# Optimization experiments

Hardware: AMD Instinct MI355X
Metric: run time of the kernel (lower is better)

## Reference

```python
import jax, jax.numpy as jnp
import numpy as np

B, S, E, H = 4, 4096, 768, 8
D = E // H  # head_dim = 96


def setup_inputs() -> dict:
    key = jax.random.key(0)
    ks = jax.random.split(key, 9)
    std = 1.0 / np.sqrt(E)
    return {
        "values": jax.random.normal(ks[0], (B, S, E), dtype=jnp.float32),
        "keys": jax.random.normal(ks[1], (B, S, E), dtype=jnp.float32),
        "query": jax.random.normal(ks[2], (B, S, E), dtype=jnp.float32),
        "mask": jax.random.randint(ks[3], (B, S, 1, 1), 0, 2, dtype=jnp.int32),
        "Wv": jax.random.normal(ks[4], (E, E), dtype=jnp.float32) * std,
        "Wk": jax.random.normal(ks[5], (E, E), dtype=jnp.float32) * std,
        "Wq": jax.random.normal(ks[6], (E, E), dtype=jnp.float32) * std,
        "Wo": jax.random.normal(ks[7], (E, E), dtype=jnp.float32) * std,
        "bo": jax.random.normal(ks[8], (E,), dtype=jnp.float32) * std,
    }


def reference(values, keys, query, mask, Wv, Wk, Wq, Wo, bo):
    b, s, e = query.shape
    h, d = H, e // H
    scale = e ** 0.5

    def split(x, W):
        # Linear (no bias) then view to [b, s, h, d] and permute to [b, h, s, d]
        return (x @ W.T).reshape(b, s, h, d).transpose(0, 2, 1, 3)

    v = split(values, Wv)   # [b, h, s, d]
    k = split(keys, Wk)     # [b, h, s, d]
    q = split(query, Wq)    # [b, h, s, d]

    # Faithful to torch.einsum('nqhd,nkhd->nhqk', q, k) with q,k laid out as
    # [b, h, s, d]: this contracts over d with s batched, producing a per-token
    # head-gram matrix att[b, s, i, j] = sum_d q[b,i,s,d] * k[b,j,s,d].
    att = jnp.einsum('bisd,bjsd->bsij', q, k)          # [b, s, h, h]
    att = jnp.where(mask == 0, jnp.float32(-1e20), att)
    att = jax.nn.softmax(att / scale, axis=3)

    # torch.einsum('nhql,nlhd->nqhd', att, v) with att [b,s,h,h], v [b,h,s,d]:
    # out[b, i, s, d] = sum_j att[b,s,i,j] * v[b,j,s,d]  -> [b, h, s, d]
    out = jnp.einsum('bsij,bjsd->bisd', att, v)        # [b, h, s, d]
    out = out.reshape(b, s, h * d)                      # row-major, matches torch .reshape
    return out @ Wo.T + bo
```

## Files before the change

kernel.cpp:

```cpp
#include <hip/hip_runtime.h>
#include <hip/hip_bf16.h>
#include <cstdint>


typedef unsigned short u16;
typedef short bf16x8 __attribute__((ext_vector_type(8)));
typedef float f32x4 __attribute__((ext_vector_type(4)));

#define B_  4
#define S_  4096
#define E_  768
#define H_  8
#define D_  96
#define T_  (B_*S_)
#define BM_ 256
#define BN_ 192

static __device__ __forceinline__ u16 f2bf(float f) {
  unsigned u = __builtin_bit_cast(unsigned, f);
  u += 0x7fffu + ((u >> 16) & 1u);
  return (u16)(u >> 16);
}
static __device__ __forceinline__ unsigned pk2(float lo, float hi) {
  return (unsigned)f2bf(lo) | ((unsigned)f2bf(hi) << 16);
}
static __device__ __forceinline__ float bflo(unsigned u) {
  return __builtin_bit_cast(float, u << 16);
}
static __device__ __forceinline__ float bfhi(unsigned u) {
  return __builtin_bit_cast(float, u & 0xffff0000u);
}

__global__ __launch_bounds__(256) void conv_bf16(
    const float* __restrict__ src, u16* __restrict__ dst)
{
  const int i = blockIdx.x * 256 + threadIdx.x;
  const float4 v = ((const float4*)src)[i];
  uint2 w;
  w.x = pk2(v.x, v.y);
  w.y = pk2(v.z, v.w);
  ((uint2*)dst)[i] = w;
}

__global__ __launch_bounds__(256) void conv_w(
    const float* __restrict__ w0, const float* __restrict__ w1,
    const float* __restrict__ w2, const float* __restrict__ w3,
    u16* __restrict__ dst)
{
  const int bpw = (E_ * E_ / 4) / 256;
  const int which = blockIdx.x / bpw;
  const float* src = which == 0 ? w0 : which == 1 ? w1 : which == 2 ? w2 : w3;
  const int i = (blockIdx.x - which * bpw) * 256 + threadIdx.x;
  const float4 v = ((const float4*)src)[i];
  uint2 w;
  w.x = pk2(v.x, v.y);
  w.y = pk2(v.z, v.w);
  ((uint2*)(dst + (size_t)which * E_ * E_))[i] = w;
}


#define GLOAD(SRC, DST)                                                        \
  __builtin_amdgcn_global_load_lds(                                            \
      (const __attribute__((address_space(1))) void*)(SRC),                    \
      (__attribute__((address_space(3))) void*)(DST), 16, 0, 0)

#define SA(BUF, I, KT) GLOAD(sA[I] + (KT), &lA[BUF][(((I) << 3) + wave) * 512])
#define SB(BUF, I, KT) GLOAD(sB[I] + (KT), &lB[BUF][(((I) << 3) + wave) * 512])

#define RDA(BUF, MH, KK, M)                                                    \
  (*(const bf16x8*)&lA[BUF][((wr << 7) + ((MH) << 6) + ((M) << 4) + l15) * 64 +\
      (((((KK) << 2) + l4) ^ (((MH) << 6) + ((M) << 4) + l15 ? ((((MH) << 6) + ((M) << 4) + l15) & 7) : 0)) << 3)])

#define MFMA12(MB)                                                             \
  {                                                                            \
    _Pragma("unroll")                                                          \
    for (int m_ = 0; m_ < 4; ++m_) {                                           \
      acc[(MB) + m_][0] = __builtin_amdgcn_mfma_f32_16x16x32_bf16(a[m_], b[0], acc[(MB) + m_][0], 0, 0, 0); \
      acc[(MB) + m_][1] = __builtin_amdgcn_mfma_f32_16x16x32_bf16(a[m_], b[1], acc[(MB) + m_][1], 0, 0, 0); \
      acc[(MB) + m_][2] = __builtin_amdgcn_mfma_f32_16x16x32_bf16(a[m_], b[2], acc[(MB) + m_][2], 0, 0, 0); \
    }                                                                          \
  }

template<bool OUT_F32, bool BIAS>
__global__ __launch_bounds__(512, 2) void gemm_big(
    const u16* __restrict__ A, const u16* __restrict__ Wt,
    const float* __restrict__ bias, void* __restrict__ Cv)
{
  __shared__ u16 lA[2][256 * 64];
  __shared__ u16 lB[2][192 * 64];
  const int tid = threadIdx.x, wave = tid >> 6, lane = tid & 63;
  const int wr = wave >> 2, wcn = wave & 3;
  const int wg = ((blockIdx.x & 7) << 5) + (blockIdx.x >> 3);
  const int tM = (wg >> 2) << 8, tN = (wg & 3) * BN_;
  const int l15 = lane & 15, l4 = lane >> 4;
  const int srow = lane >> 3;
  const int sg   = (lane & 7) ^ srow;

  const u16* sA[4];
  const u16* sB[3];
#pragma unroll
  for (int i = 0; i < 4; ++i)
    sA[i] = A + (size_t)(tM + (((i << 3) + wave) << 3) + srow) * E_ + (sg << 3);
#pragma unroll
  for (int i = 0; i < 3; ++i)
    sB[i] = Wt + (size_t)(tN + (((i << 3) + wave) << 3) + srow) * E_ + (sg << 3);

  f32x4 acc[8][3] = {};

#pragma unroll
  for (int i = 0; i < 4; ++i) SA(0, i, 0);
#pragma unroll
  for (int i = 0; i < 3; ++i) SB(0, i, 0);
  asm volatile("s_waitcnt vmcnt(0)" ::: "memory");
  __builtin_amdgcn_s_barrier();

  for (int t = 0; t < 12; ++t) {
    const int cur = t & 1, nxt = cur ^ 1;
    const int ktn = (t + 1) << 6;
    const bool pf = (t < 11);
    bf16x8 a[4], b[3];

#pragma unroll
    for (int m = 0; m < 4; ++m) {
      const int row = (wr << 7) + (m << 4) + l15;
      a[m] = *(const bf16x8*)&lA[cur][row * 64 + ((l4 ^ (row & 7)) << 3)];
    }
#pragma unroll
    for (int n = 0; n < 3; ++n) {
      const int row = wcn * 48 + (n << 4) + l15;
      b[n] = *(const bf16x8*)&lB[cur][row * 64 + ((l4 ^ (row & 7)) << 3)];
    }
    if (pf) { SA(nxt, 0, ktn); SA(nxt, 1, ktn); SA(nxt, 2, ktn); }
    __builtin_amdgcn_s_barrier();
    __builtin_amdgcn_s_setprio(1);
    MFMA12(0);
    __builtin_amdgcn_s_setprio(0);
    __builtin_amdgcn_s_barrier();

#pragma unroll
    for (int m = 0; m < 4; ++m) {
      const int row = (wr << 7) + 64 + (m << 4) + l15;
      a[m] = *(const bf16x8*)&lA[cur][row * 64 + ((l4 ^ (row & 7)) << 3)];
    }
    if (pf) { SA(nxt, 3, ktn); SB(nxt, 0, ktn); }
    __builtin_amdgcn_s_barrier();
    __builtin_amdgcn_s_setprio(1);
    MFMA12(4);
    __builtin_amdgcn_s_setprio(0);
    __builtin_amdgcn_s_barrier();

#pragma unroll
    for (int m = 0; m < 4; ++m) {
      const int row = (wr << 7) + (m << 4) + l15;
      a[m] = *(const bf16x8*)&lA[cur][row * 64 + (((4 + l4) ^ (row & 7)) << 3)];
    }
#pragma unroll
    for (int n = 0; n < 3; ++n) {
      const int row = wcn * 48 + (n << 4) + l15;
      b[n] = *(const bf16x8*)&lB[cur][row * 64 + (((4 + l4) ^ (row & 7)) << 3)];
    }
    if (pf) { SB(nxt, 1, ktn); SB(nxt, 2, ktn); }
    __builtin_amdgcn_s_barrier();
    __builtin_amdgcn_s_setprio(1);
    MFMA12(0);
    __builtin_amdgcn_s_setprio(0);
    __builtin_amdgcn_s_barrier();

#pragma unroll
    for (int m = 0; m < 4; ++m) {
      const int row = (wr << 7) + 64 + (m << 4) + l15;
      a[m] = *(const bf16x8*)&lA[cur][row * 64 + (((4 + l4) ^ (row & 7)) << 3)];
    }
    __builtin_amdgcn_s_barrier();
    __builtin_amdgcn_s_setprio(1);
    MFMA12(4);
    __builtin_amdgcn_s_setprio(0);
    if (pf) asm volatile("s_waitcnt vmcnt(0)" ::: "memory");
    __builtin_amdgcn_s_barrier();
  }

  const int cr = l4 << 2;
#pragma unroll
  for (int m = 0; m < 8; ++m) {
#pragma unroll
    for (int n = 0; n < 3; ++n) {
      const int row = tM + (wr << 7) + (m << 4) + cr;
      const int col = tN + wcn * 48 + (n << 4) + l15;
      const float badd = BIAS ? bias[col] : 0.f;
#pragma unroll
      for (int r = 0; r < 4; ++r) {
        const float val = acc[m][n][r] + badd;
        if constexpr (OUT_F32)
          ((float*)Cv)[(size_t)(row + r) * E_ + col] = val;
        else
          ((u16*)Cv)[(size_t)(row + r) * E_ + col] = f2bf(val);
      }
    }
  }
}

__global__ __launch_bounds__(256) void attn_tok(
    const u16* __restrict__ Q, const u16* __restrict__ K,
    const u16* __restrict__ V, const int* __restrict__ mask,
    u16* __restrict__ O)
{
  __shared__ float pl[4][8][8];
  const int tid = threadIdx.x, wave = tid >> 6, lane = tid & 63;
  const int t = blockIdx.x * 4 + wave;
  const int s = t & (S_ - 1);
  const int b = t >> 12;
  const int i = lane >> 3, j = lane & 7;

  const uint4* qp = (const uint4*)(Q + (size_t)t * E_ + i * D_);
  const uint4* kp = (const uint4*)(K + (size_t)t * E_ + j * D_);
  float acc = 0.f;
#pragma unroll
  for (int it = 0; it < 12; ++it) {
    const uint4 qv = qp[it], kv = kp[it];
    acc += bflo(qv.x) * bflo(kv.x) + bfhi(qv.x) * bfhi(kv.x);
    acc += bflo(qv.y) * bflo(kv.y) + bfhi(qv.y) * bfhi(kv.y);
    acc += bflo(qv.z) * bflo(kv.z) + bfhi(qv.z) * bfhi(kv.z);
    acc += bflo(qv.w) * bflo(kv.w) + bfhi(qv.w) * bfhi(kv.w);
  }
  float sv = (mask[t] == 0) ? -1e20f : acc;
  sv *= 0.03608439182435161f;
  float mx = sv;
  mx = fmaxf(mx, __shfl_xor(mx, 1));
  mx = fmaxf(mx, __shfl_xor(mx, 2));
  mx = fmaxf(mx, __shfl_xor(mx, 4));
  const float e = __expf(sv - mx);
  float sm = e;
  sm += __shfl_xor(sm, 1);
  sm += __shfl_xor(sm, 2);
  sm += __shfl_xor(sm, 4);
  pl[wave][i][j] = e / sm;
  __syncthreads();

  const int i2 = lane >> 3, db = lane & 7;
  float o[12] = {};
#pragma unroll
  for (int jj = 0; jj < 8; ++jj) {
    const float pj = pl[wave][i2][jj];
    const uint2* vp = (const uint2*)(V + (size_t)t * E_ + jj * D_ + db * 12);
    const uint2 v0 = vp[0], v1 = vp[1], v2 = vp[2];
    o[0]  += pj * bflo(v0.x);  o[1]  += pj * bfhi(v0.x);
    o[2]  += pj * bflo(v0.y);  o[3]  += pj * bfhi(v0.y);
    o[4]  += pj * bflo(v1.x);  o[5]  += pj * bfhi(v1.x);
    o[6]  += pj * bflo(v1.y);  o[7]  += pj * bfhi(v1.y);
    o[8]  += pj * bflo(v2.x);  o[9]  += pj * bfhi(v2.x);
    o[10] += pj * bflo(v2.y);  o[11] += pj * bfhi(v2.y);
  }
  const size_t row = (size_t)b * S_ + 512 * i2 + (s >> 3);
  u16* op = O + row * E_ + 96 * (s & 7) + db * 12;
  uint2 w0, w1, w2;
  w0.x = pk2(o[0], o[1]);
  w0.y = pk2(o[2], o[3]);
  w1.x = pk2(o[4], o[5]);
  w1.y = pk2(o[6], o[7]);
  w2.x = pk2(o[8], o[9]);
  w2.y = pk2(o[10], o[11]);
  ((uint2*)op)[0] = w0;
  ((uint2*)op)[1] = w1;
  ((uint2*)op)[2] = w2;
}

extern "C" void kernel_launch(void* const* d_in, const int* in_sizes, int n_in,
                              void* d_out, int out_size, void* d_ws, size_t ws_size,
                              hipStream_t stream)
{
  const float* values = (const float*)d_in[0];
  const float* keys   = (const float*)d_in[1];
  const float* query  = (const float*)d_in[2];
  const int*   mask   = (const int*)d_in[3];
  const float* Wv = (const float*)d_in[4];
  const float* Wk = (const float*)d_in[5];
  const float* Wq = (const float*)d_in[6];
  const float* Wo = (const float*)d_in[7];
  const float* bo = (const float*)d_in[8];

  const size_t TE = (size_t)T_ * E_;
  const size_t EE = (size_t)E_ * E_;
  u16* Qb = (u16*)d_ws;
  u16* Kb = Qb + TE;
  u16* Vb = Kb + TE;
  u16* Xt = Vb + TE;
  u16* Wb = Xt + TE;

  dim3 gg(T_ / BM_ * (E_ / BN_));
  dim3 gc(TE / 4 / 256);

  conv_w<<<dim3(4 * (E_ * E_ / 4) / 256), dim3(256), 0, stream>>>(Wq, Wk, Wv, Wo, Wb);

  conv_bf16<<<gc, dim3(256), 0, stream>>>(query, Xt);
  gemm_big<false, false><<<gg, dim3(512), 0, stream>>>(Xt, Wb + 0 * EE, nullptr, Qb);
  conv_bf16<<<gc, dim3(256), 0, stream>>>(keys, Xt);
  gemm_big<false, false><<<gg, dim3(512), 0, stream>>>(Xt, Wb + 1 * EE, nullptr, Kb);
  conv_bf16<<<gc, dim3(256), 0, stream>>>(values, Xt);
  gemm_big<false, false><<<gg, dim3(512), 0, stream>>>(Xt, Wb + 2 * EE, nullptr, Vb);

  attn_tok<<<dim3(T_ / 4), dim3(256), 0, stream>>>(Qb, Kb, Vb, mask, Xt );

  gemm_big<true, true><<<gg, dim3(512), 0, stream>>>(Xt , Wb + 3 * EE, bo, (float*)d_out);
}
```

Before: 184.7 us.

## Fuse fp32-to-bf16 activation conversion into projection GEMM A-tile loads

Removes the three standalone conv_bf16 passes over query/keys/values. The projection GEMMs now read fp32 activations into registers, convert them with v_cvt_pk_bf16_f32 and write swizzled bf16 into LDS. This avoids writing and re-reading a bf16 copy of each input through global memory. In exchange, the A prefetch goes through registers instead of direct global-to-LDS loads, adding register pressure and VALU/LDS-store work inside the pipelined loop.

```diff
diff --git a/kernel.cpp b/kernel.cpp
--- a/kernel.cpp
+++ b/kernel.cpp
@@ -24,22 +24,16 @@
 static __device__ __forceinline__ unsigned pk2(float lo, float hi) {
   return (unsigned)f2bf(lo) | ((unsigned)f2bf(hi) << 16);
 }
+static __device__ __forceinline__ unsigned cvtpk(float lo, float hi) {
+  unsigned r;
+  asm("v_cvt_pk_bf16_f32 %0, %1, %2" : "=v"(r) : "v"(lo), "v"(hi));
+  return r;
+}
 static __device__ __forceinline__ float bflo(unsigned u) {
   return __builtin_bit_cast(float, u << 16);
 }
 static __device__ __forceinline__ float bfhi(unsigned u) {
   return __builtin_bit_cast(float, u & 0xffff0000u);
-}
-
-__global__ __launch_bounds__(256) void conv_bf16(
-    const float* __restrict__ src, u16* __restrict__ dst)
-{
-  const int i = blockIdx.x * 256 + threadIdx.x;
-  const float4 v = ((const float4*)src)[i];
-  uint2 w;
-  w.x = pk2(v.x, v.y);
-  w.y = pk2(v.z, v.w);
-  ((uint2*)dst)[i] = w;
 }
 
 __global__ __launch_bounds__(256) void conv_w(
@@ -67,9 +61,24 @@
 #define SA(BUF, I, KT) GLOAD(sA[I] + (KT), &lA[BUF][(((I) << 3) + wave) * 512])
 #define SB(BUF, I, KT) GLOAD(sB[I] + (KT), &lB[BUF][(((I) << 3) + wave) * 512])
 
-#define RDA(BUF, MH, KK, M)                                                    \
-  (*(const bf16x8*)&lA[BUF][((wr << 7) + ((MH) << 6) + ((M) << 4) + l15) * 64 +\
-      (((((KK) << 2) + l4) ^ (((MH) << 6) + ((M) << 4) + l15 ? ((((MH) << 6) + ((M) << 4) + l15) & 7) : 0)) << 3)])
+#define A_ISSUE(KT)                                                            \
+  {                                                                            \
+    _Pragma("unroll")                                                          \
+    for (int w_ = 0; w_ < 8; ++w_)                                             \
+      av[w_] = *(const float4*)(agp + (KT) + (w_ << 2));                       \
+  }
+#define A_WRITE(BUF)                                                           \
+  {                                                                            \
+    _Pragma("unroll")                                                          \
+    for (int w_ = 0; w_ < 4; ++w_) {                                           \
+      uint4 q_;                                                                \
+      q_.x = cvtpk(av[2 * w_].x, av[2 * w_].y);                                \
+      q_.y = cvtpk(av[2 * w_].z, av[2 * w_].w);                                \
+      q_.z = cvtpk(av[2 * w_ + 1].x, av[2 * w_ + 1].y);                        \
+      q_.w = cvtpk(av[2 * w_ + 1].z, av[2 * w_ + 1].w);                        \
+      *(uint4*)&lA[BUF][ar * 64 + ((((ah << 2) + w_) ^ (ar & 7)) << 3)] = q_;  \
+    }                                                                          \
+  }
 
 #define MFMA12(MB)                                                             \
   {                                                                            \
@@ -81,9 +90,9 @@
     }                                                                          \
   }
 
-template<bool OUT_F32, bool BIAS>
+template<bool A_F32, bool OUT_F32, bool BIAS>
 __global__ __launch_bounds__(512, 2) void gemm_big(
-    const u16* __restrict__ A, const u16* __restrict__ Wt,
+    const void* __restrict__ Av, const u16* __restrict__ Wt,
     const float* __restrict__ bias, void* __restrict__ Cv)
 {
   __shared__ u16 lA[2][256 * 64];
@@ -96,23 +105,37 @@
   const int srow = lane >> 3;
   const int sg   = (lane & 7) ^ srow;
 
+  const u16* A16 = (const u16*)Av;
+  const float* A32 = (const float*)Av;
+
   const u16* sA[4];
   const u16* sB[3];
 #pragma unroll
-  for (int i = 0; i < 4; ++i)
-    sA[i] = A + (size_t)(tM + (((i << 3) + wave) << 3) + srow) * E_ + (sg << 3);
-#pragma unroll
   for (int i = 0; i < 3; ++i)
     sB[i] = Wt + (size_t)(tN + (((i << 3) + wave) << 3) + srow) * E_ + (sg << 3);
+  if constexpr (!A_F32) {
+#pragma unroll
+    for (int i = 0; i < 4; ++i)
+      sA[i] = A16 + (size_t)(tM + (((i << 3) + wave) << 3) + srow) * E_ + (sg << 3);
+  }
+  const int ar = tid >> 1, ah = tid & 1;
+  const float* agp = A32 + (size_t)(tM + ar) * E_ + (ah << 5);
 
   f32x4 acc[8][3] = {};
-
-#pragma unroll
-  for (int i = 0; i < 4; ++i) SA(0, i, 0);
-#pragma unroll
-  for (int i = 0; i < 3; ++i) SB(0, i, 0);
-  asm volatile("s_waitcnt vmcnt(0)" ::: "memory");
-  __builtin_amdgcn_s_barrier();
+  float4 av[8];
+
+  if constexpr (A_F32) {
+    A_ISSUE(0);
+#pragma unroll
+    for (int i = 0; i < 3; ++i) SB(0, i, 0);
+    A_WRITE(0);
+  } else {
+#pragma unroll
+    for (int i = 0; i < 4; ++i) SA(0, i, 0);
+#pragma unroll
+    for (int i = 0; i < 3; ++i) SB(0, i, 0);
+  }
+  __syncthreads();
 
   for (int t = 0; t < 12; ++t) {
     const int cur = t & 1, nxt = cur ^ 1;
@@ -130,7 +153,10 @@
       const int row = wcn * 48 + (n << 4) + l15;
       b[n] = *(const bf16x8*)&lB[cur][row * 64 + ((l4 ^ (row & 7)) << 3)];
     }
-    if (pf) { SA(nxt, 0, ktn); SA(nxt, 1, ktn); SA(nxt, 2, ktn); }
+    if (pf) {
+      if constexpr (A_F32) { A_ISSUE(ktn); }
+      else { SA(nxt, 0, ktn); SA(nxt, 1, ktn); SA(nxt, 2, ktn); }
+    }
     __builtin_amdgcn_s_barrier();
     __builtin_amdgcn_s_setprio(1);
     MFMA12(0);
@@ -142,7 +168,10 @@
       const int row = (wr << 7) + 64 + (m << 4) + l15;
       a[m] = *(const bf16x8*)&lA[cur][row * 64 + ((l4 ^ (row & 7)) << 3)];
     }
-    if (pf) { SA(nxt, 3, ktn); SB(nxt, 0, ktn); }
+    if (pf) {
+      if constexpr (A_F32) { SB(nxt, 0, ktn); SB(nxt, 1, ktn); SB(nxt, 2, ktn); }
+      else { SA(nxt, 3, ktn); SB(nxt, 0, ktn); }
+    }
     __builtin_amdgcn_s_barrier();
     __builtin_amdgcn_s_setprio(1);
     MFMA12(4);
@@ -159,7 +188,9 @@
       const int row = wcn * 48 + (n << 4) + l15;
       b[n] = *(const bf16x8*)&lB[cur][row * 64 + (((4 + l4) ^ (row & 7)) << 3)];
     }
-    if (pf) { SB(nxt, 1, ktn); SB(nxt, 2, ktn); }
+    if (pf) {
+      if constexpr (!A_F32) { SB(nxt, 1, ktn); SB(nxt, 2, ktn); }
+    }
     __builtin_amdgcn_s_barrier();
     __builtin_amdgcn_s_setprio(1);
     MFMA12(0);
@@ -175,7 +206,13 @@
     __builtin_amdgcn_s_setprio(1);
     MFMA12(4);
     __builtin_amdgcn_s_setprio(0);
-    if (pf) asm volatile("s_waitcnt vmcnt(0)" ::: "memory");
+    if (pf) {
+      if constexpr (A_F32) {
+        A_WRITE(nxt);
+        asm volatile("s_waitcnt lgkmcnt(0)" ::: "memory");
+      }
+      asm volatile("s_waitcnt vmcnt(0)" ::: "memory");
+    }
     __builtin_amdgcn_s_barrier();
   }
 
@@ -283,22 +320,18 @@
   u16* Qb = (u16*)d_ws;
   u16* Kb = Qb + TE;
   u16* Vb = Kb + TE;
-  u16* Xt = Vb + TE;
-  u16* Wb = Xt + TE;
+  u16* O2 = Vb + TE;
+  u16* Wb = O2 + TE;
 
   dim3 gg(T_ / BM_ * (E_ / BN_));
-  dim3 gc(TE / 4 / 256);
 
   conv_w<<<dim3(4 * (E_ * E_ / 4) / 256), dim3(256), 0, stream>>>(Wq, Wk, Wv, Wo, Wb);
 
-  conv_bf16<<<gc, dim3(256), 0, stream>>>(query, Xt);
-  gemm_big<false, false><<<gg, dim3(512), 0, stream>>>(Xt, Wb + 0 * EE, nullptr, Qb);
-  conv_bf16<<<gc, dim3(256), 0, stream>>>(keys, Xt);
-  gemm_big<false, false><<<gg, dim3(512), 0, stream>>>(Xt, Wb + 1 * EE, nullptr, Kb);
-  conv_bf16<<<gc, dim3(256), 0, stream>>>(values, Xt);
-  gemm_big<false, false><<<gg, dim3(512), 0, stream>>>(Xt, Wb + 2 * EE, nullptr, Vb);
-
-  attn_tok<<<dim3(T_ / 4), dim3(256), 0, stream>>>(Qb, Kb, Vb, mask, Xt );
-
-  gemm_big<true, true><<<gg, dim3(512), 0, stream>>>(Xt , Wb + 3 * EE, bo, (float*)d_out);
-}
+  gemm_big<true, false, false><<<gg, dim3(512), 0, stream>>>(query,  Wb + 0 * EE, nullptr, Qb);
+  gemm_big<true, false, false><<<gg, dim3(512), 0, stream>>>(keys,   Wb + 1 * EE, nullptr, Kb);
+  gemm_big<true, false, false><<<gg, dim3(512), 0, stream>>>(values, Wb + 2 * EE, nullptr, Vb);
+
+  attn_tok<<<dim3(T_ / 4), dim3(256), 0, stream>>>(Qb, Kb, Vb, mask, O2);
+
+  gemm_big<false, true, true><<<gg, dim3(512), 0, stream>>>(O2, Wb + 3 * EE, bo, (float*)d_out);
+}
```

Result: slower. 216.0 us (+16.9%).

## Rewrite projection GEMM with 256x256 tiles, quadrant pipelining and LDS-staged bf16 epilogue

Applied to the files above, without the earlier changes.

Replaces the 256x192 GEMM tile with a 256x256 tile split into four 128x128 quadrants, each wave computing 64x32 per quadrant. Global-to-LDS loads are staggered across quadrants so the next k-step's halves arrive while MFMAs run. For bf16 outputs the accumulators are staged through swizzled LDS and written as 16-byte coalesced rows instead of scattered 2-byte stores. The larger tile raises arithmetic intensity but cuts the grid to 192 blocks, which may underfill the GPU and leave CUs idle.

```diff
diff --git a/kernel.cpp b/kernel.cpp
--- a/kernel.cpp
+++ b/kernel.cpp
@@ -13,8 +13,6 @@
 #define H_  8
 #define D_  96
 #define T_  (B_*S_)
-#define BM_ 256
-#define BN_ 192
 
 static __device__ __forceinline__ u16 f2bf(float f) {
   unsigned u = __builtin_bit_cast(unsigned, f);
@@ -64,137 +62,147 @@
       (const __attribute__((address_space(1))) void*)(SRC),                    \
       (__attribute__((address_space(3))) void*)(DST), 16, 0, 0)
 
-#define SA(BUF, I, KT) GLOAD(sA[I] + (KT), &lA[BUF][(((I) << 3) + wave) * 512])
-#define SB(BUF, I, KT) GLOAD(sB[I] + (KT), &lB[BUF][(((I) << 3) + wave) * 512])
-
-#define RDA(BUF, MH, KK, M)                                                    \
-  (*(const bf16x8*)&lA[BUF][((wr << 7) + ((MH) << 6) + ((M) << 4) + l15) * 64 +\
-      (((((KK) << 2) + l4) ^ (((MH) << 6) + ((M) << 4) + l15 ? ((((MH) << 6) + ((M) << 4) + l15) & 7) : 0)) << 3)])
-
-#define MFMA12(MB)                                                             \
+#define STG_A(HALF, T)                                                         \
+  {                                                                            \
+    const int b_ = (T) & 1;                                                    \
+    GLOAD(Abase + (size_t)(tM + (HALF)*128 + (wave<<3) + srow8) * E_ + ((T)<<6) + sgo, \
+          &lds[(b_*2 + (HALF)) * 8192 + ((wave*64 + lane) << 3)]);             \
+    GLOAD(Abase + (size_t)(tM + (HALF)*128 + 64 + (wave<<3) + srow8) * E_ + ((T)<<6) + sgo, \
+          &lds[(b_*2 + (HALF)) * 8192 + (((8 + wave)*64 + lane) << 3)]);       \
+  }
+#define STG_B(HALF, T)                                                         \
+  {                                                                            \
+    const int b_ = (T) & 1;                                                    \
+    GLOAD(Wbase + (size_t)(tN + (HALF)*128 + (wave<<3) + srow8) * E_ + ((T)<<6) + sgo, \
+          &lds[32768 + (b_*2 + (HALF)) * 8192 + ((wave*64 + lane) << 3)]);     \
+    GLOAD(Wbase + (size_t)(tN + (HALF)*128 + 64 + (wave<<3) + srow8) * E_ + ((T)<<6) + sgo, \
+          &lds[32768 + (b_*2 + (HALF)) * 8192 + (((8 + wave)*64 + lane) << 3)]); \
+  }
+
+#define RD_A(DST, BUF, MH, KK)                                                 \
   {                                                                            \
     _Pragma("unroll")                                                          \
     for (int m_ = 0; m_ < 4; ++m_) {                                           \
-      acc[(MB) + m_][0] = __builtin_amdgcn_mfma_f32_16x16x32_bf16(a[m_], b[0], acc[(MB) + m_][0], 0, 0, 0); \
-      acc[(MB) + m_][1] = __builtin_amdgcn_mfma_f32_16x16x32_bf16(a[m_], b[1], acc[(MB) + m_][1], 0, 0, 0); \
-      acc[(MB) + m_][2] = __builtin_amdgcn_mfma_f32_16x16x32_bf16(a[m_], b[2], acc[(MB) + m_][2], 0, 0, 0); \
+      const int hr_ = (wr << 6) + (m_ << 4) + l15;                             \
+      DST[m_] = *(const bf16x8*)&lds[((BUF)*2 + (MH)) * 8192 + hr_ * 64 +      \
+                                     (((((KK) << 2) + l4) ^ (hr_ & 7)) << 3)]; \
     }                                                                          \
   }
+#define RD_B(DST, BUF, NH, KK)                                                 \
+  {                                                                            \
+    _Pragma("unroll")                                                          \
+    for (int n_ = 0; n_ < 2; ++n_) {                                           \
+      const int hr_ = (wcn << 5) + (n_ << 4) + l15;                            \
+      DST[n_] = *(const bf16x8*)&lds[32768 + ((BUF)*2 + (NH)) * 8192 + hr_ * 64 + \
+                                     (((((KK) << 2) + l4) ^ (hr_ & 7)) << 3)]; \
+    }                                                                          \
+  }
+
+#define MFMA16(MH, NH, B0N, B1N)                                               \
+  {                                                                            \
+    __builtin_amdgcn_s_setprio(1);                                             \
+    _Pragma("unroll")                                                          \
+    for (int m_ = 0; m_ < 4; ++m_) {                                           \
+      _Pragma("unroll")                                                        \
+      for (int n_ = 0; n_ < 2; ++n_) {                                         \
+        acc[MH][NH][m_][n_] = __builtin_amdgcn_mfma_f32_16x16x32_bf16(a0[m_], B0N[n_], acc[MH][NH][m_][n_], 0, 0, 0); \
+        acc[MH][NH][m_][n_] = __builtin_amdgcn_mfma_f32_16x16x32_bf16(a1[m_], B1N[n_], acc[MH][NH][m_][n_], 0, 0, 0); \
+      }                                                                        \
+    }                                                                          \
+    __builtin_amdgcn_s_setprio(0);                                             \
+  }
 
 template<bool OUT_F32, bool BIAS>
-__global__ __launch_bounds__(512, 2) void gemm_big(
-    const u16* __restrict__ A, const u16* __restrict__ Wt,
+__global__ __launch_bounds__(512, 2) void gemm8(
+    const u16* __restrict__ Abase, const u16* __restrict__ Wbase,
     const float* __restrict__ bias, void* __restrict__ Cv)
 {
-  __shared__ u16 lA[2][256 * 64];
-  __shared__ u16 lB[2][192 * 64];
+  __shared__ u16 lds[65536];
   const int tid = threadIdx.x, wave = tid >> 6, lane = tid & 63;
   const int wr = wave >> 2, wcn = wave & 3;
-  const int wg = ((blockIdx.x & 7) << 5) + (blockIdx.x >> 3);
-  const int tM = (wg >> 2) << 8, tN = (wg & 3) * BN_;
+  const int wg = (blockIdx.x & 7) * 24 + (blockIdx.x >> 3);
+  const int tM = (wg / 3) << 8, tN = (wg % 3) << 8;
   const int l15 = lane & 15, l4 = lane >> 4;
-  const int srow = lane >> 3;
-  const int sg   = (lane & 7) ^ srow;
-
-  const u16* sA[4];
-  const u16* sB[3];
-#pragma unroll
-  for (int i = 0; i < 4; ++i)
-    sA[i] = A + (size_t)(tM + (((i << 3) + wave) << 3) + srow) * E_ + (sg << 3);
-#pragma unroll
-  for (int i = 0; i < 3; ++i)
-    sB[i] = Wt + (size_t)(tN + (((i << 3) + wave) << 3) + srow) * E_ + (sg << 3);
-
-  f32x4 acc[8][3] = {};
-
-#pragma unroll
-  for (int i = 0; i < 4; ++i) SA(0, i, 0);
-#pragma unroll
-  for (int i = 0; i < 3; ++i) SB(0, i, 0);
-  asm volatile("s_waitcnt vmcnt(0)" ::: "memory");
+  const int srow8 = lane >> 3;
+  const int sgo = ((lane & 7) ^ srow8) << 3;
+
+  f32x4 acc[2][2][4][2] = {};
+  bf16x8 a0[4], a1[4], bh0k0[2], bh0k1[2], bh1k0[2], bh1k1[2];
+
+  STG_A(0, 0); STG_B(0, 0); STG_B(1, 0); STG_A(1, 0);
+  STG_A(0, 1); STG_B(0, 1);
+  asm volatile("s_waitcnt vmcnt(4)" ::: "memory");
   __builtin_amdgcn_s_barrier();
 
   for (int t = 0; t < 12; ++t) {
-    const int cur = t & 1, nxt = cur ^ 1;
-    const int ktn = (t + 1) << 6;
-    const bool pf = (t < 11);
-    bf16x8 a[4], b[3];
-
-#pragma unroll
-    for (int m = 0; m < 4; ++m) {
-      const int row = (wr << 7) + (m << 4) + l15;
-      a[m] = *(const bf16x8*)&lA[cur][row * 64 + ((l4 ^ (row & 7)) << 3)];
-    }
-#pragma unroll
-    for (int n = 0; n < 3; ++n) {
-      const int row = wcn * 48 + (n << 4) + l15;
-      b[n] = *(const bf16x8*)&lB[cur][row * 64 + ((l4 ^ (row & 7)) << 3)];
-    }
-    if (pf) { SA(nxt, 0, ktn); SA(nxt, 1, ktn); SA(nxt, 2, ktn); }
-    __builtin_amdgcn_s_barrier();
-    __builtin_amdgcn_s_setprio(1);
-    MFMA12(0);
-    __builtin_amdgcn_s_setprio(0);
-    __builtin_amdgcn_s_barrier();
-
-#pragma unroll
-    for (int m = 0; m < 4; ++m) {
-      const int row = (wr << 7) + 64 + (m << 4) + l15;
-      a[m] = *(const bf16x8*)&lA[cur][row * 64 + ((l4 ^ (row & 7)) << 3)];
-    }
-    if (pf) { SA(nxt, 3, ktn); SB(nxt, 0, ktn); }
-    __builtin_amdgcn_s_barrier();
-    __builtin_amdgcn_s_setprio(1);
-    MFMA12(4);
-    __builtin_amdgcn_s_setprio(0);
-    __builtin_amdgcn_s_barrier();
-
-#pragma unroll
-    for (int m = 0; m < 4; ++m) {
-      const int row = (wr << 7) + (m << 4) + l15;
-      a[m] = *(const bf16x8*)&lA[cur][row * 64 + (((4 + l4) ^ (row & 7)) << 3)];
-    }
-#pragma unroll
-    for (int n = 0; n < 3; ++n) {
-      const int row = wcn * 48 + (n << 4) + l15;
-      b[n] = *(const bf16x8*)&lB[cur][row * 64 + (((4 + l4) ^ (row & 7)) << 3)];
-    }
-    if (pf) { SB(nxt, 1, ktn); SB(nxt, 2, ktn); }
-    __builtin_amdgcn_s_barrier();
-    __builtin_amdgcn_s_setprio(1);
-    MFMA12(0);
-    __builtin_amdgcn_s_setprio(0);
-    __builtin_amdgcn_s_barrier();
-
-#pragma unroll
-    for (int m = 0; m < 4; ++m) {
-      const int row = (wr << 7) + 64 + (m << 4) + l15;
-      a[m] = *(const bf16x8*)&lA[cur][row * 64 + (((4 + l4) ^ (row & 7)) << 3)];
-    }
-    __builtin_amdgcn_s_barrier();
-    __builtin_amdgcn_s_setprio(1);
-    MFMA12(4);
-    __builtin_amdgcn_s_setprio(0);
-    if (pf) asm volatile("s_waitcnt vmcnt(0)" ::: "memory");
-    __builtin_amdgcn_s_barrier();
-  }
-
-  const int cr = l4 << 2;
-#pragma unroll
-  for (int m = 0; m < 8; ++m) {
-#pragma unroll
-    for (int n = 0; n < 3; ++n) {
-      const int row = tM + (wr << 7) + (m << 4) + cr;
-      const int col = tN + wcn * 48 + (n << 4) + l15;
-      const float badd = BIAS ? bias[col] : 0.f;
-#pragma unroll
-      for (int r = 0; r < 4; ++r) {
-        const float val = acc[m][n][r] + badd;
-        if constexpr (OUT_F32)
-          ((float*)Cv)[(size_t)(row + r) * E_ + col] = val;
-        else
-          ((u16*)Cv)[(size_t)(row + r) * E_ + col] = f2bf(val);
-      }
+    const int buf = t & 1;
+    RD_A(a0, buf, 0, 0); RD_A(a1, buf, 0, 1);
+    RD_B(bh0k0, buf, 0, 0); RD_B(bh0k1, buf, 0, 1);
+    if (t < 11) STG_B(1, t + 1);
+    __builtin_amdgcn_s_barrier();
+    MFMA16(0, 0, bh0k0, bh0k1);
+    __builtin_amdgcn_s_barrier();
+    RD_B(bh1k0, buf, 1, 0); RD_B(bh1k1, buf, 1, 1);
+    if (t < 11) STG_A(1, t + 1);
+    __builtin_amdgcn_s_barrier();
+    MFMA16(0, 1, bh1k0, bh1k1);
+    __builtin_amdgcn_s_barrier();
+    RD_A(a0, buf, 1, 0); RD_A(a1, buf, 1, 1);
+    RD_B(bh0k0, buf, 0, 0); RD_B(bh0k1, buf, 0, 1);
+    if (t < 10) STG_A(0, t + 2);
+    __builtin_amdgcn_s_barrier();
+    MFMA16(1, 0, bh0k0, bh0k1);
+    __builtin_amdgcn_s_barrier();
+    if (t < 10) STG_B(0, t + 2);
+    __builtin_amdgcn_s_barrier();
+    MFMA16(1, 1, bh1k0, bh1k1);
+    if (t < 10)       asm volatile("s_waitcnt vmcnt(4)" ::: "memory");
+    else if (t == 10) asm volatile("s_waitcnt vmcnt(0)" ::: "memory");
+    __builtin_amdgcn_s_barrier();
+  }
+
+  if constexpr (OUT_F32) {
+#pragma unroll
+    for (int mh = 0; mh < 2; ++mh)
+#pragma unroll
+      for (int nh = 0; nh < 2; ++nh)
+#pragma unroll
+        for (int m = 0; m < 4; ++m)
+#pragma unroll
+          for (int n = 0; n < 2; ++n) {
+            const int row = tM + mh * 128 + (wr << 6) + (m << 4) + (l4 << 2);
+            const int col = tN + nh * 128 + (wcn << 5) + (n << 4) + l15;
+            const float badd = BIAS ? bias[col] : 0.f;
+#pragma unroll
+            for (int r = 0; r < 4; ++r)
+              ((float*)Cv)[(size_t)(row + r) * E_ + col] = acc[mh][nh][m][n][r] + badd;
+          }
+  } else {
+    __builtin_amdgcn_s_barrier();
+#pragma unroll
+    for (int mh = 0; mh < 2; ++mh)
+#pragma unroll
+      for (int nh = 0; nh < 2; ++nh)
+#pragma unroll
+        for (int m = 0; m < 4; ++m)
+#pragma unroll
+          for (int n = 0; n < 2; ++n) {
+            const int colb = nh * 128 + (wcn << 5) + (n << 4) + l15;
+#pragma unroll
+            for (int r = 0; r < 4; ++r) {
+              const int row = mh * 128 + (wr << 6) + (m << 4) + (l4 << 2) + r;
+              const int g = colb >> 3;
+              lds[row * 256 + (((g ^ ((row & 3) << 1)) << 3) | (colb & 7))] =
+                  f2bf(acc[mh][nh][m][n][r]);
+            }
+          }
+    __builtin_amdgcn_s_barrier();
+#pragma unroll
+    for (int p = 0; p < 16; ++p) {
+      const int row = (p << 4) + (tid >> 5);
+      const int g = tid & 31;
+      const bf16x8 v = *(const bf16x8*)&lds[row * 256 + ((g ^ ((row & 3) << 1)) << 3)];
+      *(bf16x8*)((u16*)Cv + (size_t)(tM + row) * E_ + tN + (g << 3)) = v;
     }
   }
 }
@@ -286,19 +294,19 @@
   u16* Xt = Vb + TE;
   u16* Wb = Xt + TE;
 
-  dim3 gg(T_ / BM_ * (E_ / BN_));
+  dim3 gg(T_ / 256 * (E_ / 256));
   dim3 gc(TE / 4 / 256);
 
   conv_w<<<dim3(4 * (E_ * E_ / 4) / 256), dim3(256), 0, stream>>>(Wq, Wk, Wv, Wo, Wb);
 
   conv_bf16<<<gc, dim3(256), 0, stream>>>(query, Xt);
-  gemm_big<false, false><<<gg, dim3(512), 0, stream>>>(Xt, Wb + 0 * EE, nullptr, Qb);
+  gemm8<false, false><<<gg, dim3(512), 0, stream>>>(Xt, Wb + 0 * EE, nullptr, Qb);
   conv_bf16<<<gc, dim3(256), 0, stream>>>(keys, Xt);
-  gemm_big<false, false><<<gg, dim3(512), 0, stream>>>(Xt, Wb + 1 * EE, nullptr, Kb);
+  gemm8<false, false><<<gg, dim3(512), 0, stream>>>(Xt, Wb + 1 * EE, nullptr, Kb);
   conv_bf16<<<gc, dim3(256), 0, stream>>>(values, Xt);
-  gemm_big<false, false><<<gg, dim3(512), 0, stream>>>(Xt, Wb + 2 * EE, nullptr, Vb);
+  gemm8<false, false><<<gg, dim3(512), 0, stream>>>(Xt, Wb + 2 * EE, nullptr, Vb);
 
   attn_tok<<<dim3(T_ / 4), dim3(256), 0, stream>>>(Qb, Kb, Vb, mask, Xt );
 
-  gemm_big<true, true><<<gg, dim3(512), 0, stream>>>(Xt , Wb + 3 * EE, bo, (float*)d_out);
-}
+  gemm8<true, true><<<gg, dim3(512), 0, stream>>>(Xt , Wb + 3 * EE, bo, (float*)d_out);
+}
```

Measured after the change: 192.3 us. 1.04x slower.
